# Performance work log

Hardware: AMD Instinct MI355X
Metric: run time of the kernel (lower is better)

## Reference

```python
import jax, jax.numpy as jnp
import numpy as np

N_EMBED = 8192
EMBED_DIM = 256
BETA = 0.25


def setup_inputs() -> dict:
    key = jax.random.key(0)
    k1, k2 = jax.random.split(key)
    z = jax.random.normal(k1, (8, 4096, EMBED_DIM), dtype=jnp.float32)
    # original: uniform(-1/n_embed, 1/n_embed)
    embed_weight = jax.random.uniform(
        k2, (N_EMBED, EMBED_DIM), dtype=jnp.float32,
        minval=-1.0 / N_EMBED, maxval=1.0 / N_EMBED)
    return {"z": z, "embed_weight": embed_weight}


def reference(z, embed_weight):
    # z: [B, H, C] with C == embed_dim (no permute needed for this layout)
    B, H, C = z.shape
    z_flat = z.reshape(-1, C)  # [N, C]
    # squared L2 distances: ||z||^2 + ||e||^2 - 2 z e^T  -> [N, n_embed]
    d = (jnp.sum(z_flat * z_flat, axis=1, keepdims=True)
         + jnp.sum(embed_weight * embed_weight, axis=1)
         - 2.0 * jnp.matmul(z_flat, embed_weight.T))
    idx = jnp.argmin(d, axis=1)  # [N]
    z_q = embed_weight[idx].reshape(B, H, C)
    # VQ loss (stop-gradient semantics irrelevant for the forward value)
    loss = (jnp.mean((jax.lax.stop_gradient(z_q) - z) ** 2)
            + BETA * jnp.mean((z_q - jax.lax.stop_gradient(z)) ** 2))
    # straight-through estimator
    z_q_st = z + jax.lax.stop_gradient(z_q - z)
    return (z_q_st, loss, idx.reshape(B, H))
```

## Files before the change

### kernel.cpp

```cpp
#include <hip/hip_runtime.h>
#include <math.h>

#define DIM     256
#define NROWS   32768
#define NCODES  8192
#define ZQ_ELEMS (NROWS * DIM)

#define CAND_MAX 64
#define DS       2.6e-4f
#define NCB      4
#define COLS_PER_CB (NCODES / NCB)
#define BM 128
#define BN 64
#define CHUNKS (COLS_PER_CB / BN)
#define LCAP 2048

typedef __attribute__((ext_vector_type(8))) short bf16x8;
typedef __attribute__((ext_vector_type(4))) float f32x4;

__device__ __forceinline__ unsigned short bf16rne(float x) {
    unsigned u = __float_as_uint(x);
    unsigned r = (u + 0x7FFFu + ((u >> 16) & 1u)) >> 16;
    return (unsigned short)r;
}

template<int CTRL>
__device__ __forceinline__ float dppmax(float x) {
    int y = __builtin_amdgcn_update_dpp(0, __float_as_int(x), CTRL, 0xF, 0xF, false);
    return fmaxf(x, __int_as_float(y));
}
__device__ __forceinline__ float rowmax16(float x) {
    x = dppmax<0xB1>(x);
    x = dppmax<0x4E>(x);
    x = dppmax<0x141>(x);
    x = dppmax<0x140>(x);
    return x;
}

__device__ __forceinline__ float pw128_sq(const float* __restrict__ a) {
    float r[8];
#pragma unroll
    for (int j = 0; j < 8; ++j) r[j] = __fmul_rn(a[j], a[j]);
#pragma unroll
    for (int i = 8; i < 128; i += 8) {
#pragma unroll
        for (int j = 0; j < 8; ++j) r[j] = __fadd_rn(r[j], __fmul_rn(a[i + j], a[i + j]));
    }
    return __fadd_rn(__fadd_rn(__fadd_rn(r[0], r[1]), __fadd_rn(r[2], r[3])),
                     __fadd_rn(__fadd_rn(r[4], r[5]), __fadd_rn(r[6], r[7])));
}

__global__ __launch_bounds__(256) void rowsq_bf16_kernel(const float* __restrict__ src,
                                                         float* __restrict__ dst,
                                                         unsigned short* __restrict__ bdst) {
    __shared__ float tile[32][DIM + 1];
    const int row0 = blockIdx.x * 32;
    for (int e = threadIdx.x; e < 32 * DIM / 4; e += 256) {
        int r = e >> 6, c4 = e & 63;
        float4 v = *(const float4*)&src[(size_t)(row0 + r) * DIM + c4 * 4];
        tile[r][c4 * 4 + 0] = v.x; tile[r][c4 * 4 + 1] = v.y;
        tile[r][c4 * 4 + 2] = v.z; tile[r][c4 * 4 + 3] = v.w;
        ushort4 o;
        o.x = bf16rne(v.x); o.y = bf16rne(v.y); o.z = bf16rne(v.z); o.w = bf16rne(v.w);
        ((ushort4*)bdst)[(size_t)(row0 + r) * 64 + c4] = o;
    }
    __syncthreads();
    if (threadIdx.x < 32) {
        const float* a = tile[threadIdx.x];
        float s0 = pw128_sq(a);
        float s1 = pw128_sq(a + 128);
        dst[row0 + threadIdx.x] = __fadd_rn(s0, s1);
    }
}

__global__ __launch_bounds__(256) void initbuf_kernel(unsigned long long* __restrict__ keys,
                                                      int* __restrict__ cnt,
                                                      int* __restrict__ flags) {
    int t = blockIdx.x * 256 + threadIdx.x;
    keys[t] = 0xFFFFFFFFFFFFFFFFull;
    cnt[t] = 0;
    flags[t] = 0;
}

__device__ __forceinline__ void gload_lds16(const void* g, void* l) {
    __builtin_amdgcn_global_load_lds(
        (const __attribute__((address_space(1))) unsigned int*)g,
        (__attribute__((address_space(3))) unsigned int*)l, 16, 0, 0);
}

__device__ __forceinline__ void stage32k8(const char* gbase, char* lbase,
                                          int wave, int lane) {
#pragma unroll
    for (int it = 0; it < 4; ++it) {
        int ubase = it * 8192 + wave * 1024;
        int loff  = ubase + (lane << 4);
        int goff  = loff ^ (((loff >> 9) & 7) << 4);
        gload_lds16(gbase + goff, lbase + ubase);
    }
}

#define WAIT_VM4()  asm volatile("s_waitcnt vmcnt(4)" ::: "memory")
#define WAIT_VM0()  asm volatile("s_waitcnt vmcnt(0)" ::: "memory")
#define LGKM0()     asm volatile("s_waitcnt lgkmcnt(0)" ::: "memory")
#define SBAR()      __builtin_amdgcn_s_barrier()
#define SCHEDB()    __builtin_amdgcn_sched_barrier(0)

#define CHUNK_BODY(CH, ACC, LMX, PACC, PLMX)                                      \
    do {                                                                          \
        const int ch_ = (CH);                                                     \
        const char* bb = (const char*)sbuf + ((ch_ & 1) << 15);                   \
        _Pragma("unroll")                                                         \
        for (int fc = 0; fc < 4; ++fc) ACC[fc] = (f32x4){0.f, 0.f, 0.f, 0.f};     \
        __builtin_amdgcn_s_setprio(1);                                            \
        _Pragma("unroll")                                                         \
        for (int kc = 0; kc < 8; ++kc) {                                          \
            bf16x8 bfr[4];                                                        \
            _Pragma("unroll")                                                     \
            for (int fc = 0; fc < 4; ++fc)                                        \
                bfr[fc] = *(const bf16x8*)(bb +                                   \
                    ((((fc * 16 + l15) << 9) + (kc << 6) + (lg << 4)) ^ swz));    \
            _Pragma("unroll")                                                     \
            for (int fc = 0; fc < 4; ++fc)                                        \
                ACC[fc] = __builtin_amdgcn_mfma_f32_16x16x32_bf16(                \
                    afr[kc], bfr[fc], ACC[fc], 0, 0, 0);                          \
        }                                                                         \
        __builtin_amdgcn_s_setprio(0);                                            \
        LGKM0();                                                                  \
        SCHEDB();                                                                 \
        SBAR();                                                                   \
        SCHEDB();                                                                 \
        if (ch_ + 2 < CHUNKS)                                                     \
            stage32k8((const char*)(wb + ((size_t)(colbase + (ch_ + 2) * BN) << 8)), \
                      (char*)sbuf + ((ch_ & 1) << 15), wave, lane);               \
        _Pragma("unroll")                                                         \
        for (int j = 0; j < 4; ++j) {                                             \
            LMX[j] = fmaxf(fmaxf(ACC[0][j], ACC[1][j]),                           \
                           fmaxf(ACC[2][j], ACC[3][j]));                          \
            rmx[j] = fmaxf(rmx[j], rowmax16(LMX[j]));                             \
        }                                                                         \
        if (ch_ > 0) {                                                            \
            const int code0 = colbase + (ch_ - 1) * BN;                           \
            _Pragma("unroll")                                                     \
            for (int j = 0; j < 4; ++j) {                                         \
                float thr = rmx[j] - DS;                                          \
                if (PLMX[j] >= thr) {                                             \
                    const int rl = wave * 16 + lg * 4 + j;                        \
                    _Pragma("unroll")                                             \
                    for (int fc = 0; fc < 4; ++fc) {                              \
                        if (PACC[fc][j] >= thr) {                                 \
                            int code = code0 + fc * 16 + l15;                     \
                            unsigned s = atomicAdd(&lcnt, 1u);                    \
                            if (s < LCAP) {                                       \
                                list[s] = ((unsigned)rl << 13) | (unsigned)code;  \
                            } else {                                              \
                                int row = row0 + rl;                              \
                                int slot = atomicAdd(&cnt[row], 1);               \
                                if (slot < CAND_MAX)                              \
                                    cand[(size_t)row * CAND_MAX + slot] = code;   \
                                else flags[row] = 1;                              \
                            }                                                     \
                        }                                                         \
                    }                                                             \
                }                                                                 \
            }                                                                     \
        }                                                                         \
        if (ch_ + 2 < CHUNKS) { WAIT_VM4(); } else { WAIT_VM0(); }                \
        SCHEDB();                                                                 \
        SBAR();                                                                   \
        SCHEDB();                                                                 \
    } while (0)

__global__ __launch_bounds__(512, 2) void mfma_filter_kernel(
    const unsigned short* __restrict__ zb, const unsigned short* __restrict__ wb,
    int* __restrict__ cnt, int* __restrict__ cand, int* __restrict__ flags) {
    __shared__ __align__(16) unsigned short sbuf[2 * BN * DIM];
    __shared__ unsigned list[LCAP];
    __shared__ unsigned lcnt;

    const int tid  = threadIdx.x;
    const int wave = tid >> 6;
    const int lane = tid & 63;
    const int l15 = lane & 15, lg = lane >> 4;
    const int bid = blockIdx.x;
    const int r8  = bid & 7;
    const int cb  = r8 >> 1;
    const int rb  = ((bid >> 3) << 1) | (r8 & 1);
    const int row0 = rb * BM;
    const int colbase = cb * COLS_PER_CB;
    const int swz = (l15 & 7) << 4;

    if (tid == 0) lcnt = 0;

    bf16x8 afr[8];
    const unsigned short* za = zb + (size_t)(row0 + wave * 16 + l15) * DIM + lg * 8;
#pragma unroll
    for (int kc = 0; kc < 8; ++kc)
        afr[kc] = __builtin_nontemporal_load((const bf16x8*)(za + kc * 32));
    SCHEDB();

    stage32k8((const char*)(wb + ((size_t)colbase << 8)), (char*)sbuf, wave, lane);
    stage32k8((const char*)(wb + ((size_t)(colbase + BN) << 8)),
              (char*)sbuf + 32768, wave, lane);
    LGKM0();
    WAIT_VM4();
    SCHEDB();
    SBAR();
    SCHEDB();

    float rmx[4];
#pragma unroll
    for (int j = 0; j < 4; ++j) rmx[j] = -INFINITY;

    f32x4 accE[4], accO[4];
    float lmxE[4], lmxO[4];

#pragma unroll 1
    for (int p = 0; p < CHUNKS; p += 2) {
        CHUNK_BODY(p,     accE, lmxE, accO, lmxO);
        CHUNK_BODY(p + 1, accO, lmxO, accE, lmxE);
    }

    {
        const int code0 = colbase + (CHUNKS - 1) * BN;
#pragma unroll
        for (int j = 0; j < 4; ++j) {
            float thr = rmx[j] - DS;
            if (lmxO[j] >= thr) {
                const int rl = wave * 16 + lg * 4 + j;
#pragma unroll
                for (int fc = 0; fc < 4; ++fc) {
                    if (accO[fc][j] >= thr) {
                        int code = code0 + fc * 16 + l15;
                        unsigned s = atomicAdd(&lcnt, 1u);
                        if (s < LCAP) {
                            list[s] = ((unsigned)rl << 13) | (unsigned)code;
                        } else {
                            int row = row0 + rl;
                            int slot = atomicAdd(&cnt[row], 1);
                            if (slot < CAND_MAX)
                                cand[(size_t)row * CAND_MAX + slot] = code;
                            else flags[row] = 1;
                        }
                    }
                }
            }
        }
    }

    LGKM0();
    SCHEDB();
    SBAR();
    SCHEDB();
    unsigned n = lcnt;
    if (n > LCAP) n = LCAP;
    for (unsigned i = tid; i < n; i += 512) {
        unsigned e = list[i];
        int rl = (int)(e >> 13);
        int code = (int)(e & 8191u);
        int row = row0 + rl;
        int slot = atomicAdd(&cnt[row], 1);
        if (slot < CAND_MAX) cand[(size_t)row * CAND_MAX + slot] = code;
        else flags[row] = 1;
    }
}

__device__ __forceinline__ float exact_dot(const float* __restrict__ zr,
                                           const float* __restrict__ wj) {
    const f32x4* z4 = (const f32x4*)zr;
    const f32x4* w4 = (const f32x4*)wj;
    float m = 0.0f;
#pragma unroll 8
    for (int k4 = 0; k4 < 64; ++k4) {
        f32x4 a = z4[k4], b = w4[k4];
        m = fmaf(a[0], b[0], m);
        m = fmaf(a[1], b[1], m);
        m = fmaf(a[2], b[2], m);
        m = fmaf(a[3], b[3], m);
    }
    return m;
}

__global__ __launch_bounds__(256) void recheck_kernel(
    const float* __restrict__ z, const float* __restrict__ w,
    const float* __restrict__ P, const float* __restrict__ Q,
    const int* __restrict__ cnt, const int* __restrict__ cand,
    const int* __restrict__ flags, unsigned long long* __restrict__ keys) {
    const int gid  = blockIdx.x * 256 + threadIdx.x;
    const int row  = gid >> 6;
    const int slot = gid & 63;
    const float* zr = z + (size_t)row * DIM;

    if (flags[row]) {
        for (int j = slot; j < NCODES; j += 64) {
            float m = exact_dot(zr, w + (size_t)j * DIM);
            float d = __fsub_rn(__fadd_rn(P[row], Q[j]), __fmul_rn(2.0f, m));
            unsigned long long key =
                ((unsigned long long)__float_as_uint(d) << 32) | (unsigned)j;
            atomicMin(&keys[row], key);
        }
        return;
    }
    int n = cnt[row]; if (n > CAND_MAX) n = CAND_MAX;
    if (slot >= n) return;
    const int j = cand[(size_t)row * CAND_MAX + slot];
    float m = exact_dot(zr, w + (size_t)j * DIM);
    float d = __fsub_rn(__fadd_rn(P[row], Q[j]), __fmul_rn(2.0f, m));
    unsigned long long key = ((unsigned long long)__float_as_uint(d) << 32) | (unsigned)j;
    atomicMin(&keys[row], key);
}

__global__ __launch_bounds__(256) void finalize_kernel(
    const unsigned long long* __restrict__ keys,
    int* __restrict__ idx_i, float* __restrict__ idx_f) {
    int r = blockIdx.x * 256 + threadIdx.x;
    int j = (int)(unsigned)(keys[r] & 0xFFFFFFFFull);
    idx_i[r] = j;
    idx_f[r] = (float)j;
}

__global__ __launch_bounds__(256) void gather_loss_kernel(
    const float* __restrict__ z, const float* __restrict__ w,
    const int* __restrict__ idx_i, float* __restrict__ zq_out,
    double* __restrict__ partial) {
    __shared__ double red[256];
    const int t    = blockIdx.x * 256 + threadIdx.x;
    const int base = t * 4;
    const int row  = base >> 8;
    const int c    = base & 255;
    const int code = idx_i[row];
    f32x4 zv = __builtin_nontemporal_load((const f32x4*)&z[base]);
    f32x4 wv = *(const f32x4*)&w[(size_t)code * DIM + c];
    float o[4];
    double s = 0.0;
#pragma unroll
    for (int j = 0; j < 4; ++j) {
        float diff = __fsub_rn(wv[j], zv[j]);
        o[j] = __fadd_rn(zv[j], diff);
        double dd = (double)diff;
        s += dd * dd;
    }
    f32x4 ov = { o[0], o[1], o[2], o[3] };
    __builtin_nontemporal_store(ov, (f32x4*)&zq_out[base]);
    red[threadIdx.x] = s;
    __syncthreads();
    for (int st = 128; st > 0; st >>= 1) {
        if (threadIdx.x < st) red[threadIdx.x] += red[threadIdx.x + st];
        __syncthreads();
    }
    if (threadIdx.x == 0) partial[blockIdx.x] = red[0];
}

__global__ __launch_bounds__(256) void loss_final_kernel(const double* __restrict__ partial,
                                                         float* __restrict__ loss_out) {
    __shared__ double red[256];
    double s = 0.0;
    for (int i = threadIdx.x; i < 8192; i += 256) s += partial[i];
    red[threadIdx.x] = s;
    __syncthreads();
    for (int st = 128; st > 0; st >>= 1) {
        if (threadIdx.x < st) red[threadIdx.x] += red[threadIdx.x + st];
        __syncthreads();
    }
    if (threadIdx.x == 0)
        loss_out[0] = (float)(1.25 * red[0] / (double)ZQ_ELEMS);
}

#define FB_BM 128
#define FB_BN 128
#define FB_BK 32
#define FB_PITCH 132

__global__ __launch_bounds__(256, 4) void vq_partial_kernel(
    const float* __restrict__ z, const float* __restrict__ w,
    const float* __restrict__ P, const float* __restrict__ Q,
    float* __restrict__ cand_d, int* __restrict__ cand_i) {
    __shared__ float As[FB_BK][FB_PITCH];
    __shared__ float Bs[FB_BK][FB_PITCH];
    const int tid  = threadIdx.x;
    const int rb   = blockIdx.x >> 2;
    const int cb   = blockIdx.x & 3;
    const int row0 = rb * FB_BM;
    const int colbase = cb * COLS_PER_CB;
    const int rg = tid >> 4;
    const int cg = tid & 15;
    float Pr[8];
#pragma unroll
    for (int i = 0; i < 8; ++i) Pr[i] = P[row0 + rg * 8 + i];
    float bestD[8]; int bestI[8];
#pragma unroll
    for (int i = 0; i < 8; ++i) { bestD[i] = INFINITY; bestI[i] = 0; }
    for (int ct = 0; ct < COLS_PER_CB; ct += FB_BN) {
        const int c0 = colbase + ct;
        float acc[8][8];
#pragma unroll
        for (int i = 0; i < 8; ++i)
#pragma unroll
            for (int j = 0; j < 8; ++j) acc[i][j] = 0.0f;
        for (int kc = 0; kc < DIM; kc += FB_BK) {
            __syncthreads();
#pragma unroll
            for (int it = 0; it < 4; ++it) {
                int u = it * 256 + tid;
                int r = u >> 3, kg = u & 7;
                float4 a = *(const float4*)&z[(size_t)(row0 + r) * DIM + kc + kg * 4];
                As[kg * 4 + 0][r] = a.x; As[kg * 4 + 1][r] = a.y;
                As[kg * 4 + 2][r] = a.z; As[kg * 4 + 3][r] = a.w;
                float4 b = *(const float4*)&w[(size_t)(c0 + r) * DIM + kc + kg * 4];
                Bs[kg * 4 + 0][r] = b.x; Bs[kg * 4 + 1][r] = b.y;
                Bs[kg * 4 + 2][r] = b.z; Bs[kg * 4 + 3][r] = b.w;
            }
            __syncthreads();
#pragma unroll
            for (int k = 0; k < FB_BK; ++k) {
                float av[8], bv[8];
                { float4 t = *(const float4*)&As[k][rg * 8];
                  av[0]=t.x; av[1]=t.y; av[2]=t.z; av[3]=t.w; }
                { float4 t = *(const float4*)&As[k][rg * 8 + 4];
                  av[4]=t.x; av[5]=t.y; av[6]=t.z; av[7]=t.w; }
                { float4 t = *(const float4*)&Bs[k][cg * 4];
                  bv[0]=t.x; bv[1]=t.y; bv[2]=t.z; bv[3]=t.w; }
                { float4 t = *(const float4*)&Bs[k][cg * 4 + 64];
                  bv[4]=t.x; bv[5]=t.y; bv[6]=t.z; bv[7]=t.w; }
#pragma unroll
                for (int i = 0; i < 8; ++i)
#pragma unroll
                    for (int j = 0; j < 8; ++j)
                        acc[i][j] = fmaf(av[i], bv[j], acc[i][j]);
            }
        }
        float qv[8];
        { float4 t = *(const float4*)&Q[c0 + cg * 4];
          qv[0]=t.x; qv[1]=t.y; qv[2]=t.z; qv[3]=t.w; }
        { float4 t = *(const float4*)&Q[c0 + 64 + cg * 4];
          qv[4]=t.x; qv[5]=t.y; qv[6]=t.z; qv[7]=t.w; }
#pragma unroll
        for (int i = 0; i < 8; ++i)
#pragma unroll
            for (int j = 0; j < 8; ++j) {
                float d = __fsub_rn(__fadd_rn(Pr[i], qv[j]), __fmul_rn(2.0f, acc[i][j]));
                int code = c0 + ((j < 4) ? (cg * 4 + j) : (64 + cg * 4 + (j - 4)));
                if (d < bestD[i]) { bestD[i] = d; bestI[i] = code; }
            }
    }
#pragma unroll
    for (int off = 1; off < 16; off <<= 1)
#pragma unroll
        for (int i = 0; i < 8; ++i) {
            float od = __shfl_xor(bestD[i], off);
            int   oi = __shfl_xor(bestI[i], off);
            if (od < bestD[i] || (od == bestD[i] && oi < bestI[i])) {
                bestD[i] = od; bestI[i] = oi;
            }
        }
    if (cg == 0)
#pragma unroll
        for (int i = 0; i < 8; ++i) {
            int row = row0 + rg * 8 + i;
            cand_d[cb * NROWS + row] = bestD[i];
            cand_i[cb * NROWS + row] = bestI[i];
        }
}

__global__ __launch_bounds__(256) void argmin_reduce_kernel(
    const float* __restrict__ cand_d, const int* __restrict__ cand_i,
    int* __restrict__ idx_i, float* __restrict__ idx_f) {
    const int row = blockIdx.x * 256 + threadIdx.x;
    float bd = cand_d[row];
    int   bi = cand_i[row];
#pragma unroll
    for (int cb = 1; cb < NCB; ++cb) {
        float d = cand_d[cb * NROWS + row];
        int   ii = cand_i[cb * NROWS + row];
        if (d < bd || (d == bd && ii < bi)) { bd = d; bi = ii; }
    }
    idx_i[row] = bi;
    idx_f[row] = (float)bi;
}

extern "C" void kernel_launch(void* const* d_in, const int* in_sizes, int n_in,
                              void* d_out, int out_size, void* d_ws, size_t ws_size,
                              hipStream_t stream) {
    const float* z = (const float*)d_in[0];
    const float* w = (const float*)d_in[1];
    float* out = (float*)d_out;

    float* ws = (float*)d_ws;
    unsigned short* zb = (unsigned short*)ws;
    unsigned short* wb = (unsigned short*)(ws + 4194304);
    float*  P       = ws + 4194304 + 1048576;
    float*  Q       = P + NROWS;
    int*    idx_i   = (int*)(Q + NCODES);
    double* partial = (double*)(idx_i + NROWS);
    unsigned long long* keys = (unsigned long long*)(partial + 8192);
    int*    cnt     = (int*)(keys + NROWS);
    int*    flags   = cnt + NROWS;
    int*    cand    = flags + NROWS;
    const size_t NEED = ((size_t)(4194304 + 1048576 + 32768 + 8192 + 32768 + 16384 + 65536
                                  + 32768 + 32768 + 2097152)) * 4;

    if (ws_size >= NEED) {
        rowsq_bf16_kernel<<<NROWS / 32, 256, 0, stream>>>(z, P, zb);
        rowsq_bf16_kernel<<<NCODES / 32, 256, 0, stream>>>(w, Q, wb);
        initbuf_kernel<<<NROWS / 256, 256, 0, stream>>>(keys, cnt, flags);
        mfma_filter_kernel<<<(NROWS / BM) * NCB, 512, 0, stream>>>(zb, wb, cnt, cand, flags);
        recheck_kernel<<<NROWS * CAND_MAX / 256, 256, 0, stream>>>(z, w, P, Q, cnt, cand,
                                                                   flags, keys);
        finalize_kernel<<<NROWS / 256, 256, 0, stream>>>(keys, idx_i, out + ZQ_ELEMS + 1);
    } else {
        rowsq_bf16_kernel<<<NROWS / 32, 256, 0, stream>>>(z, P, zb);
        rowsq_bf16_kernel<<<NCODES / 32, 256, 0, stream>>>(w, Q, wb);
        float* cand_d = (float*)(partial + 8192);
        int*   cand_i = (int*)(cand_d + NCB * NROWS);
        vq_partial_kernel<<<(NROWS / FB_BM) * NCB, 256, 0, stream>>>(z, w, P, Q, cand_d, cand_i);
        argmin_reduce_kernel<<<NROWS / 256, 256, 0, stream>>>(cand_d, cand_i, idx_i,
                                                              out + ZQ_ELEMS + 1);
    }

    gather_loss_kernel<<<ZQ_ELEMS / (256 * 4), 256, 0, stream>>>(z, w, idx_i, out, partial);
    loss_final_kernel<<<1, 256, 0, stream>>>(partial, out + ZQ_ELEMS);
}
```

Baseline: 572.9 us.

## Retile MFMA filter to 256 threads with 32-row waves and fuse small kernels

The MFMA filter kernel now uses 4 waves per block, each covering 32 rows (two A fragments) against 32-code chunks. That halves the LDS stage size and raises the occupancy target to 4 blocks per CU. The init kernel is folded into the z row-norm kernel, and the finalize kernel is folded into gather_loss, which reads indices straight from the packed keys. The recheck kernel uses 32 threads per row and loops over candidates. The aim is to cut launch overhead and improve B-fragment reuse and latency hiding, at the cost of more barriers per code and higher register pressure.

```diff
diff --git a/kernel.cpp b/kernel.cpp
--- a/kernel.cpp
+++ b/kernel.cpp
@@ -11,9 +11,9 @@
 #define NCB      4
 #define COLS_PER_CB (NCODES / NCB)
 #define BM 128
-#define BN 64
+#define BN 32
 #define CHUNKS (COLS_PER_CB / BN)
-#define LCAP 2048
+#define LCAP 1792
 
 typedef __attribute__((ext_vector_type(8))) short bf16x8;
 typedef __attribute__((ext_vector_type(4))) float f32x4;
@@ -52,9 +52,18 @@
 
 __global__ __launch_bounds__(256) void rowsq_bf16_kernel(const float* __restrict__ src,
                                                          float* __restrict__ dst,
-                                                         unsigned short* __restrict__ bdst) {
+                                                         unsigned short* __restrict__ bdst,
+                                                         unsigned long long* __restrict__ keys,
+                                                         int* __restrict__ cnt,
+                                                         int* __restrict__ flags) {
     __shared__ float tile[32][DIM + 1];
     const int row0 = blockIdx.x * 32;
+    if (keys != nullptr && blockIdx.x < 128) {
+        int gid = blockIdx.x * 256 + threadIdx.x;
+        keys[gid] = 0xFFFFFFFFFFFFFFFFull;
+        cnt[gid] = 0;
+        flags[gid] = 0;
+    }
     for (int e = threadIdx.x; e < 32 * DIM / 4; e += 256) {
         int r = e >> 6, c4 = e & 63;
         float4 v = *(const float4*)&src[(size_t)(row0 + r) * DIM + c4 * 4];
@@ -73,26 +82,17 @@
     }
 }
 
-__global__ __launch_bounds__(256) void initbuf_kernel(unsigned long long* __restrict__ keys,
-                                                      int* __restrict__ cnt,
-                                                      int* __restrict__ flags) {
-    int t = blockIdx.x * 256 + threadIdx.x;
-    keys[t] = 0xFFFFFFFFFFFFFFFFull;
-    cnt[t] = 0;
-    flags[t] = 0;
-}
-
 __device__ __forceinline__ void gload_lds16(const void* g, void* l) {
     __builtin_amdgcn_global_load_lds(
         (const __attribute__((address_space(1))) unsigned int*)g,
         (__attribute__((address_space(3))) unsigned int*)l, 16, 0, 0);
 }
 
-__device__ __forceinline__ void stage32k8(const char* gbase, char* lbase,
-                                          int wave, int lane) {
+__device__ __forceinline__ void stage16k(const char* gbase, char* lbase,
+                                         int wave, int lane) {
 #pragma unroll
     for (int it = 0; it < 4; ++it) {
-        int ubase = it * 8192 + wave * 1024;
+        int ubase = it * 4096 + wave * 1024;
         int loff  = ubase + (lane << 4);
         int goff  = loff ^ (((loff >> 9) & 7) << 4);
         gload_lds16(gbase + goff, lbase + ubase);
@@ -108,21 +108,25 @@
 #define CHUNK_BODY(CH, ACC, LMX, PACC, PLMX)                                      \
     do {                                                                          \
         const int ch_ = (CH);                                                     \
-        const char* bb = (const char*)sbuf + ((ch_ & 1) << 15);                   \
+        const char* bb = (const char*)sbuf + ((ch_ & 1) << 14);                   \
         _Pragma("unroll")                                                         \
-        for (int fc = 0; fc < 4; ++fc) ACC[fc] = (f32x4){0.f, 0.f, 0.f, 0.f};     \
+        for (int fr = 0; fr < 2; ++fr)                                            \
+            _Pragma("unroll")                                                     \
+            for (int fc = 0; fc < 2; ++fc) ACC[fr][fc] = (f32x4){0.f,0.f,0.f,0.f};\
         __builtin_amdgcn_s_setprio(1);                                            \
         _Pragma("unroll")                                                         \
         for (int kc = 0; kc < 8; ++kc) {                                          \
-            bf16x8 bfr[4];                                                        \
+            bf16x8 bfr[2];                                                        \
             _Pragma("unroll")                                                     \
-            for (int fc = 0; fc < 4; ++fc)                                        \
+            for (int fc = 0; fc < 2; ++fc)                                        \
                 bfr[fc] = *(const bf16x8*)(bb +                                   \
                     ((((fc * 16 + l15) << 9) + (kc << 6) + (lg << 4)) ^ swz));    \
             _Pragma("unroll")                                                     \
-            for (int fc = 0; fc < 4; ++fc)                                        \
-                ACC[fc] = __builtin_amdgcn_mfma_f32_16x16x32_bf16(                \
-                    afr[kc], bfr[fc], ACC[fc], 0, 0, 0);                          \
+            for (int fr = 0; fr < 2; ++fr)                                        \
+                _Pragma("unroll")                                                 \
+                for (int fc = 0; fc < 2; ++fc)                                    \
+                    ACC[fr][fc] = __builtin_amdgcn_mfma_f32_16x16x32_bf16(        \
+                        afr[fr][kc], bfr[fc], ACC[fr][fc], 0, 0, 0);              \
         }                                                                         \
         __builtin_amdgcn_s_setprio(0);                                            \
         LGKM0();                                                                  \
@@ -130,39 +134,42 @@
         SBAR();                                                                   \
         SCHEDB();                                                                 \
         if (ch_ + 2 < CHUNKS)                                                     \
-            stage32k8((const char*)(wb + ((size_t)(colbase + (ch_ + 2) * BN) << 8)), \
-                      (char*)sbuf + ((ch_ & 1) << 15), wave, lane);               \
+            stage16k((const char*)(wb + ((size_t)(colbase + (ch_ + 2) * BN) << 8)), \
+                     (char*)sbuf + ((ch_ & 1) << 14), wave, lane);                \
         _Pragma("unroll")                                                         \
-        for (int j = 0; j < 4; ++j) {                                             \
-            LMX[j] = fmaxf(fmaxf(ACC[0][j], ACC[1][j]),                           \
-                           fmaxf(ACC[2][j], ACC[3][j]));                          \
-            rmx[j] = fmaxf(rmx[j], rowmax16(LMX[j]));                             \
-        }                                                                         \
+        for (int fr = 0; fr < 2; ++fr)                                            \
+            _Pragma("unroll")                                                     \
+            for (int j = 0; j < 4; ++j) {                                         \
+                LMX[fr][j] = fmaxf(ACC[fr][0][j], ACC[fr][1][j]);                 \
+                rmx[fr][j] = fmaxf(rmx[fr][j], rowmax16(LMX[fr][j]));             \
+            }                                                                     \
         if (ch_ > 0) {                                                            \
             const int code0 = colbase + (ch_ - 1) * BN;                           \
             _Pragma("unroll")                                                     \
-            for (int j = 0; j < 4; ++j) {                                         \
-                float thr = rmx[j] - DS;                                          \
-                if (PLMX[j] >= thr) {                                             \
-                    const int rl = wave * 16 + lg * 4 + j;                        \
-                    _Pragma("unroll")                                             \
-                    for (int fc = 0; fc < 4; ++fc) {                              \
-                        if (PACC[fc][j] >= thr) {                                 \
-                            int code = code0 + fc * 16 + l15;                     \
-                            unsigned s = atomicAdd(&lcnt, 1u);                    \
-                            if (s < LCAP) {                                       \
-                                list[s] = ((unsigned)rl << 13) | (unsigned)code;  \
-                            } else {                                              \
-                                int row = row0 + rl;                              \
-                                int slot = atomicAdd(&cnt[row], 1);               \
-                                if (slot < CAND_MAX)                              \
-                                    cand[(size_t)row * CAND_MAX + slot] = code;   \
-                                else flags[row] = 1;                              \
+            for (int fr = 0; fr < 2; ++fr)                                        \
+                _Pragma("unroll")                                                 \
+                for (int j = 0; j < 4; ++j) {                                     \
+                    float thr = rmx[fr][j] - DS;                                  \
+                    if (PLMX[fr][j] >= thr) {                                     \
+                        const int rl = wave * 32 + fr * 16 + lg * 4 + j;          \
+                        _Pragma("unroll")                                         \
+                        for (int fc = 0; fc < 2; ++fc) {                          \
+                            if (PACC[fr][fc][j] >= thr) {                         \
+                                int code = code0 + fc * 16 + l15;                 \
+                                unsigned s = atomicAdd(&lcnt, 1u);                \
+                                if (s < LCAP) {                                   \
+                                    list[s] = ((unsigned)rl << 13) | (unsigned)code; \
+                                } else {                                          \
+                                    int row = row0 + rl;                          \
+                                    int slot = atomicAdd(&cnt[row], 1);           \
+                                    if (slot < CAND_MAX)                          \
+                                        cand[(size_t)row * CAND_MAX + slot] = code; \
+                                    else flags[row] = 1;                          \
+                                }                                                 \
                             }                                                     \
                         }                                                         \
                     }                                                             \
                 }                                                                 \
-            }                                                                     \
         }                                                                         \
         if (ch_ + 2 < CHUNKS) { WAIT_VM4(); } else { WAIT_VM0(); }                \
         SCHEDB();                                                                 \
@@ -170,7 +177,7 @@
         SCHEDB();                                                                 \
     } while (0)
 
-__global__ __launch_bounds__(512, 2) void mfma_filter_kernel(
+__global__ __launch_bounds__(256, 4) void mfma_filter_kernel(
     const unsigned short* __restrict__ zb, const unsigned short* __restrict__ wb,
     int* __restrict__ cnt, int* __restrict__ cand, int* __restrict__ flags) {
     __shared__ __align__(16) unsigned short sbuf[2 * BN * DIM];
@@ -191,28 +198,33 @@
 
     if (tid == 0) lcnt = 0;
 
-    bf16x8 afr[8];
-    const unsigned short* za = zb + (size_t)(row0 + wave * 16 + l15) * DIM + lg * 8;
-#pragma unroll
-    for (int kc = 0; kc < 8; ++kc)
-        afr[kc] = __builtin_nontemporal_load((const bf16x8*)(za + kc * 32));
+    bf16x8 afr[2][8];
+    const unsigned short* za = zb + (size_t)(row0 + wave * 32 + l15) * DIM + lg * 8;
+#pragma unroll
+    for (int fr = 0; fr < 2; ++fr)
+#pragma unroll
+        for (int kc = 0; kc < 8; ++kc)
+            afr[fr][kc] = __builtin_nontemporal_load(
+                (const bf16x8*)(za + (size_t)fr * 16 * DIM + kc * 32));
     SCHEDB();
 
-    stage32k8((const char*)(wb + ((size_t)colbase << 8)), (char*)sbuf, wave, lane);
-    stage32k8((const char*)(wb + ((size_t)(colbase + BN) << 8)),
-              (char*)sbuf + 32768, wave, lane);
+    stage16k((const char*)(wb + ((size_t)colbase << 8)), (char*)sbuf, wave, lane);
+    stage16k((const char*)(wb + ((size_t)(colbase + BN) << 8)),
+             (char*)sbuf + 16384, wave, lane);
     LGKM0();
     WAIT_VM4();
     SCHEDB();
     SBAR();
     SCHEDB();
 
-    float rmx[4];
-#pragma unroll
-    for (int j = 0; j < 4; ++j) rmx[j] = -INFINITY;
-
-    f32x4 accE[4], accO[4];
-    float lmxE[4], lmxO[4];
+    float rmx[2][4];
+#pragma unroll
+    for (int fr = 0; fr < 2; ++fr)
+#pragma unroll
+        for (int j = 0; j < 4; ++j) rmx[fr][j] = -INFINITY;
+
+    f32x4 accE[2][2], accO[2][2];
+    float lmxE[2][4], lmxO[2][4];
 
 #pragma unroll 1
     for (int p = 0; p < CHUNKS; p += 2) {
@@ -223,28 +235,30 @@
     {
         const int code0 = colbase + (CHUNKS - 1) * BN;
 #pragma unroll
-        for (int j = 0; j < 4; ++j) {
-            float thr = rmx[j] - DS;
-            if (lmxO[j] >= thr) {
-                const int rl = wave * 16 + lg * 4 + j;
-#pragma unroll
-                for (int fc = 0; fc < 4; ++fc) {
-                    if (accO[fc][j] >= thr) {
-                        int code = code0 + fc * 16 + l15;
-                        unsigned s = atomicAdd(&lcnt, 1u);
-                        if (s < LCAP) {
-                            list[s] = ((unsigned)rl << 13) | (unsigned)code;
-                        } else {
-                            int row = row0 + rl;
-                            int slot = atomicAdd(&cnt[row], 1);
-                            if (slot < CAND_MAX)
-                                cand[(size_t)row * CAND_MAX + slot] = code;
-                            else flags[row] = 1;
+        for (int fr = 0; fr < 2; ++fr)
+#pragma unroll
+            for (int j = 0; j < 4; ++j) {
+                float thr = rmx[fr][j] - DS;
+                if (lmxO[fr][j] >= thr) {
+                    const int rl = wave * 32 + fr * 16 + lg * 4 + j;
+#pragma unroll
+                    for (int fc = 0; fc < 2; ++fc) {
+                        if (accO[fr][fc][j] >= thr) {
+                            int code = code0 + fc * 16 + l15;
+                            unsigned s = atomicAdd(&lcnt, 1u);
+                            if (s < LCAP) {
+                                list[s] = ((unsigned)rl << 13) | (unsigned)code;
+                            } else {
+                                int row = row0 + rl;
+                                int slot = atomicAdd(&cnt[row], 1);
+                                if (slot < CAND_MAX)
+                                    cand[(size_t)row * CAND_MAX + slot] = code;
+                                else flags[row] = 1;
+                            }
                         }
                     }
                 }
             }
-        }
     }
 
     LGKM0();
@@ -253,7 +267,7 @@
     SCHEDB();
     unsigned n = lcnt;
     if (n > LCAP) n = LCAP;
-    for (unsigned i = tid; i < n; i += 512) {
+    for (unsigned i = tid; i < n; i += 256) {
         unsigned e = list[i];
         int rl = (int)(e >> 13);
         int code = (int)(e & 8191u);
@@ -286,12 +300,12 @@
     const int* __restrict__ cnt, const int* __restrict__ cand,
     const int* __restrict__ flags, unsigned long long* __restrict__ keys) {
     const int gid  = blockIdx.x * 256 + threadIdx.x;
-    const int row  = gid >> 6;
-    const int slot = gid & 63;
+    const int row  = gid >> 5;
+    const int slot = gid & 31;
     const float* zr = z + (size_t)row * DIM;
 
     if (flags[row]) {
-        for (int j = slot; j < NCODES; j += 64) {
+        for (int j = slot; j < NCODES; j += 32) {
             float m = exact_dot(zr, w + (size_t)j * DIM);
             float d = __fsub_rn(__fadd_rn(P[row], Q[j]), __fmul_rn(2.0f, m));
             unsigned long long key =
@@ -301,33 +315,29 @@
         return;
     }
     int n = cnt[row]; if (n > CAND_MAX) n = CAND_MAX;
-    if (slot >= n) return;
-    const int j = cand[(size_t)row * CAND_MAX + slot];
-    float m = exact_dot(zr, w + (size_t)j * DIM);
-    float d = __fsub_rn(__fadd_rn(P[row], Q[j]), __fmul_rn(2.0f, m));
-    unsigned long long key = ((unsigned long long)__float_as_uint(d) << 32) | (unsigned)j;
-    atomicMin(&keys[row], key);
-}
-
-__global__ __launch_bounds__(256) void finalize_kernel(
-    const unsigned long long* __restrict__ keys,
-    int* __restrict__ idx_i, float* __restrict__ idx_f) {
-    int r = blockIdx.x * 256 + threadIdx.x;
-    int j = (int)(unsigned)(keys[r] & 0xFFFFFFFFull);
-    idx_i[r] = j;
-    idx_f[r] = (float)j;
+    for (int s = slot; s < n; s += 32) {
+        const int j = cand[(size_t)row * CAND_MAX + s];
+        float m = exact_dot(zr, w + (size_t)j * DIM);
+        float d = __fsub_rn(__fadd_rn(P[row], Q[j]), __fmul_rn(2.0f, m));
+        unsigned long long key = ((unsigned long long)__float_as_uint(d) << 32) | (unsigned)j;
+        atomicMin(&keys[row], key);
+    }
 }
 
 __global__ __launch_bounds__(256) void gather_loss_kernel(
     const float* __restrict__ z, const float* __restrict__ w,
-    const int* __restrict__ idx_i, float* __restrict__ zq_out,
+    const unsigned long long* __restrict__ keys, const int* __restrict__ idx_i,
+    float* __restrict__ zq_out, float* __restrict__ idx_f,
     double* __restrict__ partial) {
     __shared__ double red[256];
     const int t    = blockIdx.x * 256 + threadIdx.x;
     const int base = t * 4;
     const int row  = base >> 8;
     const int c    = base & 255;
-    const int code = idx_i[row];
+    int code;
+    if (keys != nullptr) code = (int)(unsigned)(keys[row] & 0xFFFFFFFFull);
+    else                 code = idx_i[row];
+    if (c == 0) idx_f[row] = (float)code;
     f32x4 zv = __builtin_nontemporal_load((const f32x4*)&z[base]);
     f32x4 wv = *(const f32x4*)&w[(size_t)code * DIM + c];
     float o[4];
@@ -499,23 +509,24 @@
                                   + 32768 + 32768 + 2097152)) * 4;
 
     if (ws_size >= NEED) {
-        rowsq_bf16_kernel<<<NROWS / 32, 256, 0, stream>>>(z, P, zb);
-        rowsq_bf16_kernel<<<NCODES / 32, 256, 0, stream>>>(w, Q, wb);
-        initbuf_kernel<<<NROWS / 256, 256, 0, stream>>>(keys, cnt, flags);
-        mfma_filter_kernel<<<(NROWS / BM) * NCB, 512, 0, stream>>>(zb, wb, cnt, cand, flags);
-        recheck_kernel<<<NROWS * CAND_MAX / 256, 256, 0, stream>>>(z, w, P, Q, cnt, cand,
-                                                                   flags, keys);
-        finalize_kernel<<<NROWS / 256, 256, 0, stream>>>(keys, idx_i, out + ZQ_ELEMS + 1);
+        rowsq_bf16_kernel<<<NROWS / 32, 256, 0, stream>>>(z, P, zb, keys, cnt, flags);
+        rowsq_bf16_kernel<<<NCODES / 32, 256, 0, stream>>>(w, Q, wb, nullptr, nullptr, nullptr);
+        mfma_filter_kernel<<<(NROWS / BM) * NCB, 256, 0, stream>>>(zb, wb, cnt, cand, flags);
+        recheck_kernel<<<NROWS * 32 / 256, 256, 0, stream>>>(z, w, P, Q, cnt, cand,
+                                                             flags, keys);
+        gather_loss_kernel<<<ZQ_ELEMS / (256 * 4), 256, 0, stream>>>(
+            z, w, keys, nullptr, out, out + ZQ_ELEMS + 1, partial);
     } else {
-        rowsq_bf16_kernel<<<NROWS / 32, 256, 0, stream>>>(z, P, zb);
-        rowsq_bf16_kernel<<<NCODES / 32, 256, 0, stream>>>(w, Q, wb);
+        rowsq_bf16_kernel<<<NROWS / 32, 256, 0, stream>>>(z, P, zb, nullptr, nullptr, nullptr);
+        rowsq_bf16_kernel<<<NCODES / 32, 256, 0, stream>>>(w, Q, wb, nullptr, nullptr, nullptr);
         float* cand_d = (float*)(partial + 8192);
         int*   cand_i = (int*)(cand_d + NCB * NROWS);
         vq_partial_kernel<<<(NROWS / FB_BM) * NCB, 256, 0, stream>>>(z, w, P, Q, cand_d, cand_i);
         argmin_reduce_kernel<<<NROWS / 256, 256, 0, stream>>>(cand_d, cand_i, idx_i,
                                                               out + ZQ_ELEMS + 1);
-    }
-
-    gather_loss_kernel<<<ZQ_ELEMS / (256 * 4), 256, 0, stream>>>(z, w, idx_i, out, partial);
+        gather_loss_kernel<<<ZQ_ELEMS / (256 * 4), 256, 0, stream>>>(
+            z, w, nullptr, idx_i, out, out + ZQ_ELEMS + 1, partial);
+    }
+
     loss_final_kernel<<<1, 256, 0, stream>>>(partial, out + ZQ_ELEMS);
 }
```

Result: slower. 945.9 us (+65.1%).
